# Performance work log

Hardware: AMD Instinct MI355X
Metric: run time of the kernel (lower is better)

The kernel has to match this reference:

```python
import jax, jax.numpy as jnp
import numpy as np

N_NODES = 100000
N_EDGES = 1600000
N_GRAPHS = 256
K_HOPS = 3


def setup_inputs() -> dict:
    key = jax.random.key(0)
    ks = jax.random.split(key, 10)
    x = jax.random.normal(ks[0], (N_NODES, 32), dtype=jnp.float32)
    edge_index = jax.random.randint(ks[1], (2, N_EDGES), 0, N_NODES, dtype=jnp.int32)
    batch = jnp.sort(jax.random.randint(ks[2], (N_NODES,), 0, N_GRAPHS, dtype=jnp.int32))
    gcn_w = jax.random.normal(ks[3], (64, 32), dtype=jnp.float32) * 0.1
    gcn_b = jax.random.normal(ks[4], (64,), dtype=jnp.float32) * 0.1
    w1 = jax.random.normal(ks[5], (32, 64), dtype=jnp.float32) * 0.1
    b1 = jax.random.normal(ks[6], (32,), dtype=jnp.float32) * 0.1
    w2 = jax.random.normal(ks[7], (16, 32), dtype=jnp.float32) * 0.1
    b2 = jax.random.normal(ks[8], (16,), dtype=jnp.float32) * 0.1
    return {"x": x, "edge_index": edge_index, "batch": batch,
            "gcn_w": gcn_w, "gcn_b": gcn_b, "w1": w1, "b1": b1, "w2": w2, "b2": b2}


def reference(x, edge_index, batch, gcn_w, gcn_b, w1, b1, w2, b2):
    N = x.shape[0]
    src, dst = edge_index[0], edge_index[1]
    # GCN symmetric normalization with self-loops: deg = in-degree + 1
    deg = jax.ops.segment_sum(jnp.ones_like(src, dtype=x.dtype), dst, num_segments=N) + 1.0
    norm = deg ** -0.5  # [N]
    h = x
    for _ in range(K_HOPS):
        # edge message: norm[src] * h[src], scattered to dst, scaled by norm[dst];
        # self-loop contributes norm[i]^2 * h[i]
        msg = h[src] * norm[src][:, None]                     # [E, C]
        agg = jax.ops.segment_sum(msg, dst, num_segments=N)    # [N, C]
        h = norm[:, None] * agg + (norm * norm)[:, None] * h
    h = jax.nn.relu(h @ gcn_w.T + gcn_b)                       # [N, hidden]
    # global mean pool per graph
    counts = jax.ops.segment_sum(jnp.ones((N,), x.dtype), batch, num_segments=N_GRAPHS)
    sums = jax.ops.segment_sum(h, batch, num_segments=N_GRAPHS)
    h_avg = sums / jnp.maximum(counts, 1.0)[:, None]           # [G, hidden]
    # classifier (dropout = identity in eval)
    h1 = jax.nn.relu(h_avg @ w1.T + b1)
    logits = h1 @ w2.T + b2                                    # [G, nc]
    return logits
```

## Files before the change

### kernel.cpp

```cpp
#include <hip/hip_runtime.h>

constexpr int NW    = 391;
constexpr int CH    = 8192;
constexpr int CAP_B = 8192;
constexpr int CAP_C = 10240;

__device__ __forceinline__ unsigned bf16_rne(float x) {
    unsigned u = __float_as_uint(x);
    u += 0x7fffu + ((u >> 16) & 1u);
    return u >> 16;
}
__device__ __forceinline__ unsigned pack2(float even, float odd) {
    return bf16_rne(even) | (bf16_rne(odd) << 16);
}
__device__ __forceinline__ float lo_f(unsigned u) { return __uint_as_float(u << 16); }
__device__ __forceinline__ float hi_f(unsigned u) { return __uint_as_float(u & 0xffff0000u); }


__global__ __launch_bounds__(512) void k_bucket(const int* __restrict__ src,
                                                const int* __restrict__ dst, int E,
                                                int* __restrict__ wcur, int* __restrict__ packed) {
    __shared__ int h[256];
    __shared__ int base[256];
    int t = threadIdx.x;
    if (t < 256) h[t] = 0;
    __syncthreads();
    int b0 = blockIdx.x * CH;
    int cnt = min(CH, E - b0);
    if (cnt == CH) {
        const int4* d4 = (const int4*)(dst + b0);
        for (int i = t; i < CH / 4; i += 512) {
            int4 v = d4[i];
            atomicAdd(&h[v.x / NW], 1); atomicAdd(&h[v.y / NW], 1);
            atomicAdd(&h[v.z / NW], 1); atomicAdd(&h[v.w / NW], 1);
        }
    } else {
        for (int i = t; i < cnt; i += 512) atomicAdd(&h[dst[b0 + i] / NW], 1);
    }
    __syncthreads();
    if (t < 256) { base[t] = atomicAdd(&wcur[t], h[t]); h[t] = 0; }
    __syncthreads();
    if (cnt == CH) {
        const int4* d4 = (const int4*)(dst + b0);
        const int4* s4 = (const int4*)(src + b0);
        for (int i = t; i < CH / 4; i += 512) {
            int4 dv = d4[i];
            int4 sv = s4[i];
            int da[4] = {dv.x, dv.y, dv.z, dv.w};
            int sa[4] = {sv.x, sv.y, sv.z, sv.w};
#pragma unroll
            for (int j = 0; j < 4; ++j) {
                int w = da[j] / NW;
                int l = da[j] - w * NW;
                int r = atomicAdd(&h[w], 1);
                int pos = base[w] + r;
                if (pos < CAP_B) packed[w * CAP_B + pos] = (l << 17) | sa[j];
            }
        }
    } else {
        for (int i = t; i < cnt; i += 512) {
            int d = dst[b0 + i];
            int s = src[b0 + i];
            int w = d / NW;
            int l = d - w * NW;
            int r = atomicAdd(&h[w], 1);
            int pos = base[w] + r;
            if (pos < CAP_B) packed[w * CAP_B + pos] = (l << 17) | s;
        }
    }
}


__global__ __launch_bounds__(512) void k_window(const int* __restrict__ packed,
                                                const int* __restrict__ wcur,
                                                const float4* __restrict__ x4,
                                                float* __restrict__ norm,
                                                int2* __restrict__ rng,
                                                int* __restrict__ csr,
                                                uint2* __restrict__ hb, int N, int W) {
    __shared__ int hist[NW];
    __shared__ float snorm[NW];
    __shared__ int pend[NW];
    __shared__ int cur[NW];
    __shared__ int wpart[8];
    int t = threadIdx.x, w = blockIdx.x;
    int lo = w * NW, nwn = min(NW, N - lo);
    for (int i = t; i < NW; i += 512) hist[i] = 0;
    __syncthreads();
    int cnt = min(wcur[w], CAP_B);
    const int* pk = packed + (size_t)w * CAP_B;
    for (int e = t; e < cnt; e += 512) atomicAdd(&hist[pk[e] >> 17], 1);
    __syncthreads();
    int d = (t < nwn) ? hist[t] : 0;
    float nv = rsqrtf((float)(d + 1));
    if (t < nwn) { snorm[t] = nv; norm[lo + t] = nv; }
    int pd = (t < nwn) ? ((d + 7) & ~7) : 0;
    int lane = t & 63, wid = t >> 6;
    int v = pd;
#pragma unroll
    for (int s = 1; s < 64; s <<= 1) {
        int u = __shfl_up(v, s, 64);
        if (lane >= s) v += u;
    }
    if (lane == 63) wpart[wid] = v;
    __syncthreads();
    if (t < 8) {
        int z = wpart[t];
#pragma unroll
        for (int s = 1; s < 8; s <<= 1) {
            int u = __shfl_up(z, s, 8);
            if (t >= s) z += u;
        }
        wpart[t] = z;
    }
    __syncthreads();
    int incl = v + (wid ? wpart[wid - 1] : 0);
    int base = w * CAP_C;
    int cend = base + incl;
    if (t < nwn) {
        rng[lo + t] = make_int2(cend - pd, cend);
        pend[t] = cend;
        cur[t] = cend - pd;
    }
    if (w == W - 1 && t == 0) { norm[N] = 1.f; rng[N] = make_int2(0, 0); }
    __syncthreads();
    for (int e = t; e < cnt; e += 512) {
        int p = pk[e];
        int pos = atomicAdd(&cur[p >> 17], 1);
        csr[pos] = p & 0x1FFFF;
    }
    __syncthreads();
    if (t < nwn) {
        for (int pos = cur[t]; pos < pend[t]; ++pos) csr[pos] = N;
    }
    for (int idx = t; idx < nwn * 8; idx += 512) {
        int node = idx >> 3, q = idx & 7;
        float nn = snorm[node];
        float4 vx = x4[(size_t)(lo + node) * 8 + q];
        hb[(size_t)(lo + node) * 8 + q] =
            make_uint2(pack2(vx.x * nn, vx.y * nn), pack2(vx.z * nn, vx.w * nn));
    }
    if (w == W - 1 && t < 8) hb[(size_t)N * 8 + t] = make_uint2(0u, 0u);
}

template <bool LAST>
__global__ __launch_bounds__(256) void k_hop(const uint4* __restrict__ tab4,
                                             const float* __restrict__ norm,
                                             const int2* __restrict__ rng,
                                             const int* __restrict__ csr,
                                             uint4* __restrict__ out4, int N) {
    int gid = blockIdx.x * blockDim.x + threadIdx.x;
    int group = gid >> 2;
    int l = threadIdx.x & 3;
    if (group > N) return;
    uint4 sv = tab4[(size_t)group * 4 + l];
    float a0 = lo_f(sv.x), a1 = hi_f(sv.x), a2 = lo_f(sv.y), a3 = hi_f(sv.y);
    float a4 = lo_f(sv.z), a5 = hi_f(sv.z), a6 = lo_f(sv.w), a7 = hi_f(sv.w);
    int2 be = rng[group];
    for (int k = be.x; k < be.y; k += 8) {
        int2 ev = *(const int2*)(csr + k + 2 * l);
        uint4 u[8];
#pragma unroll
        for (int j = 0; j < 8; ++j) {
            int s = __shfl((j & 1) ? ev.y : ev.x, j >> 1, 4);
            u[j] = tab4[(size_t)s * 4 + l];
        }
#pragma unroll
        for (int j = 0; j < 8; ++j) {
            a0 += lo_f(u[j].x); a1 += hi_f(u[j].x); a2 += lo_f(u[j].y); a3 += hi_f(u[j].y);
            a4 += lo_f(u[j].z); a5 += hi_f(u[j].z); a6 += lo_f(u[j].w); a7 += hi_f(u[j].w);
        }
    }
    float n = norm[group];
    float sc = LAST ? n : n * n;
    out4[(size_t)group * 4 + l] = make_uint4(pack2(a0 * sc, a1 * sc), pack2(a2 * sc, a3 * sc),
                                             pack2(a4 * sc, a5 * sc), pack2(a6 * sc, a7 * sc));
}


__global__ __launch_bounds__(256) void k_feat(const uint2* __restrict__ hb,
                                              const float* __restrict__ gw,
                                              const float* __restrict__ gb,
                                              uint4* __restrict__ zb4, int N) {
    __shared__ float w[64 * 32];
    __shared__ float bs[64];
    int t = threadIdx.x;
    for (int i = t; i < 64 * 32; i += 256) w[i] = gw[i];
    if (t < 64) bs[t] = gb[t];
    __syncthreads();
    int n = blockIdx.x * 256 + t;
    if (n >= N) return;
    float hrow[32];
    const uint2* hr = hb + (size_t)n * 8;
#pragma unroll
    for (int q = 0; q < 8; ++q) {
        uint2 u = hr[q];
        hrow[q * 4] = lo_f(u.x); hrow[q * 4 + 1] = hi_f(u.x);
        hrow[q * 4 + 2] = lo_f(u.y); hrow[q * 4 + 3] = hi_f(u.y);
    }
#pragma unroll
    for (int c0 = 0; c0 < 64; c0 += 16) {
        float o[16];
#pragma unroll
        for (int cc = 0; cc < 16; ++cc) {
            const float* wr = &w[(c0 + cc) * 32];
            float d = bs[c0 + cc];
#pragma unroll
            for (int k = 0; k < 32; ++k) d += hrow[k] * wr[k];
            o[cc] = fmaxf(d, 0.f);
        }
        zb4[(size_t)n * 8 + (c0 >> 3)] =
            make_uint4(pack2(o[0], o[1]), pack2(o[2], o[3]), pack2(o[4], o[5]), pack2(o[6], o[7]));
        zb4[(size_t)n * 8 + (c0 >> 3) + 1] =
            make_uint4(pack2(o[8], o[9]), pack2(o[10], o[11]), pack2(o[12], o[13]), pack2(o[14], o[15]));
    }
}


__global__ __launch_bounds__(256) void k_pool(const uint2* __restrict__ zb2,
                                              const int* __restrict__ batch, int N,
                                              const float* __restrict__ w1, const float* __restrict__ b1,
                                              const float* __restrict__ w2, const float* __restrict__ b2,
                                              float* __restrict__ out) {
    __shared__ float4 part[16][17];
    __shared__ float havg[64];
    __shared__ float h1s[32];
    __shared__ int se[2];
    int t = threadIdx.x, g = blockIdx.x;
    if (t < 2) {
        int target = g + t;
        int lo = 0, hi = N;
        while (lo < hi) { int mid = (lo + hi) >> 1; if (batch[mid] < target) lo = mid + 1; else hi = mid; }
        se[t] = lo;
    }
    __syncthreads();
    int start = se[0], end = se[1];
    int q = t & 15;
    int r = t >> 4;
    float4 acc = make_float4(0.f, 0.f, 0.f, 0.f);
    for (int n = start + r; n < end; n += 16) {
        uint2 v = zb2[(size_t)n * 16 + q];
        acc.x += lo_f(v.x); acc.y += hi_f(v.x); acc.z += lo_f(v.y); acc.w += hi_f(v.y);
    }
    part[r][q] = acc;
    __syncthreads();
#pragma unroll
    for (int s = 8; s > 0; s >>= 1) {
        if (r < s) {
            float4 a = part[r][q], b = part[r + s][q];
            a.x += b.x; a.y += b.y; a.z += b.z; a.w += b.w;
            part[r][q] = a;
        }
        __syncthreads();
    }
    if (t < 16) {
        int cnt = end - start;
        float inv = 1.f / (float)(cnt > 0 ? cnt : 1);
        float4 a = part[0][t];
        havg[t * 4] = a.x * inv; havg[t * 4 + 1] = a.y * inv;
        havg[t * 4 + 2] = a.z * inv; havg[t * 4 + 3] = a.w * inv;
    }
    __syncthreads();
    if (t < 32) {
        float d = b1[t];
#pragma unroll
        for (int k = 0; k < 64; ++k) d += havg[k] * w1[t * 64 + k];
        h1s[t] = fmaxf(d, 0.f);
    }
    __syncthreads();
    if (t < 16) {
        float d = b2[t];
#pragma unroll
        for (int j = 0; j < 32; ++j) d += h1s[j] * w2[t * 32 + j];
        out[g * 16 + t] = d;
    }
}


extern "C" void kernel_launch(void* const* d_in, const int* in_sizes, int n_in,
                              void* d_out, int out_size, void* d_ws, size_t ws_size,
                              hipStream_t stream) {
    const float* x     = (const float*)d_in[0];
    const int*   ei    = (const int*)d_in[1];
    const int*   batch = (const int*)d_in[2];
    const float* gw    = (const float*)d_in[3];
    const float* gb    = (const float*)d_in[4];
    const float* w1    = (const float*)d_in[5];
    const float* b1    = (const float*)d_in[6];
    const float* w2    = (const float*)d_in[7];
    const float* b2    = (const float*)d_in[8];
    float* out = (float*)d_out;

    int N = in_sizes[2];
    int E = in_sizes[1] / 2;
    int G = out_size / 16;
    const int* srcp = ei;
    const int* dstp = ei + E;

    int W  = (N + NW - 1) / NW;
    int NB = (E + CH - 1) / CH;

    char* ws = (char*)d_ws;
    size_t off = 0;
    auto alloc = [&](size_t bytes) -> void* {
        void* p = ws + off;
        off += (bytes + 255) & ~(size_t)255;
        return p;
    };
    int*   wcur   = (int*)alloc(256 * 4);
    int*   packed = (int*)alloc((size_t)W * CAP_B * 4);
    int*   csr    = (int*)alloc((size_t)W * CAP_C * 4);
    int2*  rng    = (int2*)alloc((size_t)(N + 1) * 8);
    float* norm   = (float*)alloc((size_t)(N + 1) * 4);
    uint2* hbA    = (uint2*)alloc((size_t)(N + 1) * 64);
    uint2* hbB    = (uint2*)alloc((size_t)(N + 1) * 64);
    unsigned* zbuf = (unsigned*)alloc((size_t)N * 64 * 2);

    hipMemsetAsync(wcur, 0, 256 * 4, stream);

    int hb_blocks = ((N + 1) * 4 + 255) / 256;

    k_bucket<<<NB, 512, 0, stream>>>(srcp, dstp, E, wcur, packed);
    k_window<<<W, 512, 0, stream>>>(packed, wcur, (const float4*)x, norm, rng, csr, hbA, N, W);

    k_hop<false><<<hb_blocks, 256, 0, stream>>>((const uint4*)hbA, norm, rng, csr, (uint4*)hbB, N);
    k_hop<false><<<hb_blocks, 256, 0, stream>>>((const uint4*)hbB, norm, rng, csr, (uint4*)hbA, N);
    k_hop<true ><<<hb_blocks, 256, 0, stream>>>((const uint4*)hbA, norm, rng, csr, (uint4*)hbB, N);

    k_feat<<<(N + 255) / 256, 256, 0, stream>>>(hbB, gw, gb, (uint4*)zbuf, N);
    k_pool<<<G, 256, 0, stream>>>((const uint2*)zbuf, batch, N, w1, b1, w2, b2, out);
}
```

Baseline: 211.5 us.

## Use 8 lanes per node in hop gathers and fuse last hop with GCN linear

```diff
diff --git a/kernel.cpp b/kernel.cpp
--- a/kernel.cpp
+++ b/kernel.cpp
@@ -143,76 +143,131 @@
     if (w == W - 1 && t < 8) hb[(size_t)N * 8 + t] = make_uint2(0u, 0u);
 }
 
-template <bool LAST>
-__global__ __launch_bounds__(256) void k_hop(const uint4* __restrict__ tab4,
-                                             const float* __restrict__ norm,
-                                             const int2* __restrict__ rng,
-                                             const int* __restrict__ csr,
-                                             uint4* __restrict__ out4, int N) {
-    int gid = blockIdx.x * blockDim.x + threadIdx.x;
-    int group = gid >> 2;
-    int l = threadIdx.x & 3;
+__global__ void k_hop(const uint2* __restrict__ tab, const float* __restrict__ norm,
+                      const int2* __restrict__ rng, const int* __restrict__ csr,
+                      uint2* __restrict__ outb, int N) {
+    int group = (blockIdx.x * blockDim.x + threadIdx.x) >> 3;
+    int l = threadIdx.x & 7;
     if (group > N) return;
-    uint4 sv = tab4[(size_t)group * 4 + l];
-    float a0 = lo_f(sv.x), a1 = hi_f(sv.x), a2 = lo_f(sv.y), a3 = hi_f(sv.y);
-    float a4 = lo_f(sv.z), a5 = hi_f(sv.z), a6 = lo_f(sv.w), a7 = hi_f(sv.w);
+    uint2 sv = tab[(size_t)group * 8 + l];
+    float ax = lo_f(sv.x), ay = hi_f(sv.x), az = lo_f(sv.y), aw = hi_f(sv.y);
     int2 be = rng[group];
-    for (int k = be.x; k < be.y; k += 8) {
-        int2 ev = *(const int2*)(csr + k + 2 * l);
-        uint4 u[8];
+    int k = be.x;
+    for (; k + 16 <= be.y; k += 16) {
+        int e0 = csr[k + l];
+        int e1 = csr[k + 8 + l];
+        uint2 u[16];
 #pragma unroll
         for (int j = 0; j < 8; ++j) {
-            int s = __shfl((j & 1) ? ev.y : ev.x, j >> 1, 4);
-            u[j] = tab4[(size_t)s * 4 + l];
+            int s = __shfl(e0, j, 8);
+            u[j] = tab[(size_t)s * 8 + l];
         }
 #pragma unroll
         for (int j = 0; j < 8; ++j) {
-            a0 += lo_f(u[j].x); a1 += hi_f(u[j].x); a2 += lo_f(u[j].y); a3 += hi_f(u[j].y);
-            a4 += lo_f(u[j].z); a5 += hi_f(u[j].z); a6 += lo_f(u[j].w); a7 += hi_f(u[j].w);
+            int s = __shfl(e1, j, 8);
+            u[8 + j] = tab[(size_t)s * 8 + l];
+        }
+#pragma unroll
+        for (int j = 0; j < 16; ++j) {
+            ax += lo_f(u[j].x); ay += hi_f(u[j].x);
+            az += lo_f(u[j].y); aw += hi_f(u[j].y);
+        }
+    }
+    if (k < be.y) {
+        int e = csr[k + l];
+        uint2 u[8];
+#pragma unroll
+        for (int j = 0; j < 8; ++j) {
+            int s = __shfl(e, j, 8);
+            u[j] = tab[(size_t)s * 8 + l];
+        }
+#pragma unroll
+        for (int j = 0; j < 8; ++j) {
+            ax += lo_f(u[j].x); ay += hi_f(u[j].x);
+            az += lo_f(u[j].y); aw += hi_f(u[j].y);
         }
     }
     float n = norm[group];
-    float sc = LAST ? n : n * n;
-    out4[(size_t)group * 4 + l] = make_uint4(pack2(a0 * sc, a1 * sc), pack2(a2 * sc, a3 * sc),
-                                             pack2(a4 * sc, a5 * sc), pack2(a6 * sc, a7 * sc));
-}
-
-
-__global__ __launch_bounds__(256) void k_feat(const uint2* __restrict__ hb,
-                                              const float* __restrict__ gw,
-                                              const float* __restrict__ gb,
-                                              uint4* __restrict__ zb4, int N) {
-    __shared__ float w[64 * 32];
+    float sc = n * n;
+    outb[(size_t)group * 8 + l] = make_uint2(pack2(ax * sc, ay * sc), pack2(az * sc, aw * sc));
+}
+
+__global__ __launch_bounds__(256) void k_hopfeat(const uint2* __restrict__ tab,
+                                                 const float* __restrict__ norm,
+                                                 const int2* __restrict__ rng,
+                                                 const int* __restrict__ csr,
+                                                 const float* __restrict__ gw,
+                                                 const float* __restrict__ gb,
+                                                 uint4* __restrict__ zb4, int N) {
+    __shared__ float wT[32][64];
     __shared__ float bs[64];
+    __shared__ float rows[32][33];
     int t = threadIdx.x;
-    for (int i = t; i < 64 * 32; i += 256) w[i] = gw[i];
+    for (int i = t; i < 64 * 32; i += 256) { int c = i >> 5, k = i & 31; wT[k][c] = gw[i]; }
     if (t < 64) bs[t] = gb[t];
-    __syncthreads();
-    int n = blockIdx.x * 256 + t;
-    if (n >= N) return;
-    float hrow[32];
-    const uint2* hr = hb + (size_t)n * 8;
-#pragma unroll
-    for (int q = 0; q < 8; ++q) {
-        uint2 u = hr[q];
-        hrow[q * 4] = lo_f(u.x); hrow[q * 4 + 1] = hi_f(u.x);
-        hrow[q * 4 + 2] = lo_f(u.y); hrow[q * 4 + 3] = hi_f(u.y);
-    }
-#pragma unroll
-    for (int c0 = 0; c0 < 64; c0 += 16) {
-        float o[16];
-#pragma unroll
-        for (int cc = 0; cc < 16; ++cc) {
-            const float* wr = &w[(c0 + cc) * 32];
+    int group = (blockIdx.x * 256 + t) >> 3;
+    int l = t & 7;
+    int node = t >> 3;
+    float ax = 0.f, ay = 0.f, az = 0.f, aw = 0.f;
+    if (group <= N) {
+        uint2 sv = tab[(size_t)group * 8 + l];
+        ax = lo_f(sv.x); ay = hi_f(sv.x); az = lo_f(sv.y); aw = hi_f(sv.y);
+        int2 be = rng[group];
+        int k = be.x;
+        for (; k + 16 <= be.y; k += 16) {
+            int e0 = csr[k + l];
+            int e1 = csr[k + 8 + l];
+            uint2 u[16];
+#pragma unroll
+            for (int j = 0; j < 8; ++j) {
+                int s = __shfl(e0, j, 8);
+                u[j] = tab[(size_t)s * 8 + l];
+            }
+#pragma unroll
+            for (int j = 0; j < 8; ++j) {
+                int s = __shfl(e1, j, 8);
+                u[8 + j] = tab[(size_t)s * 8 + l];
+            }
+#pragma unroll
+            for (int j = 0; j < 16; ++j) {
+                ax += lo_f(u[j].x); ay += hi_f(u[j].x);
+                az += lo_f(u[j].y); aw += hi_f(u[j].y);
+            }
+        }
+        if (k < be.y) {
+            int e = csr[k + l];
+            uint2 u[8];
+#pragma unroll
+            for (int j = 0; j < 8; ++j) {
+                int s = __shfl(e, j, 8);
+                u[j] = tab[(size_t)s * 8 + l];
+            }
+#pragma unroll
+            for (int j = 0; j < 8; ++j) {
+                ax += lo_f(u[j].x); ay += hi_f(u[j].x);
+                az += lo_f(u[j].y); aw += hi_f(u[j].y);
+            }
+        }
+        float n = norm[group];
+        ax *= n; ay *= n; az *= n; aw *= n;
+    }
+    rows[node][l * 4 + 0] = ax;
+    rows[node][l * 4 + 1] = ay;
+    rows[node][l * 4 + 2] = az;
+    rows[node][l * 4 + 3] = aw;
+    __syncthreads();
+    if (group < N) {
+        int c0 = l * 8;
+        float o[8];
+#pragma unroll
+        for (int cc = 0; cc < 8; ++cc) {
             float d = bs[c0 + cc];
 #pragma unroll
-            for (int k = 0; k < 32; ++k) d += hrow[k] * wr[k];
+            for (int k = 0; k < 32; ++k) d += rows[node][k] * wT[k][c0 + cc];
             o[cc] = fmaxf(d, 0.f);
         }
-        zb4[(size_t)n * 8 + (c0 >> 3)] =
+        zb4[(size_t)group * 8 + l] =
             make_uint4(pack2(o[0], o[1]), pack2(o[2], o[3]), pack2(o[4], o[5]), pack2(o[6], o[7]));
-        zb4[(size_t)n * 8 + (c0 >> 3) + 1] =
-            make_uint4(pack2(o[8], o[9]), pack2(o[10], o[11]), pack2(o[12], o[13]), pack2(o[14], o[15]));
     }
 }
 
@@ -318,15 +373,14 @@
 
     hipMemsetAsync(wcur, 0, 256 * 4, stream);
 
-    int hb_blocks = ((N + 1) * 4 + 255) / 256;
+    int pb = ((N + 1) * 8 + 255) / 256;
 
     k_bucket<<<NB, 512, 0, stream>>>(srcp, dstp, E, wcur, packed);
     k_window<<<W, 512, 0, stream>>>(packed, wcur, (const float4*)x, norm, rng, csr, hbA, N, W);
 
-    k_hop<false><<<hb_blocks, 256, 0, stream>>>((const uint4*)hbA, norm, rng, csr, (uint4*)hbB, N);
-    k_hop<false><<<hb_blocks, 256, 0, stream>>>((const uint4*)hbB, norm, rng, csr, (uint4*)hbA, N);
-    k_hop<true ><<<hb_blocks, 256, 0, stream>>>((const uint4*)hbA, norm, rng, csr, (uint4*)hbB, N);
-
-    k_feat<<<(N + 255) / 256, 256, 0, stream>>>(hbB, gw, gb, (uint4*)zbuf, N);
+    k_hop<<<pb, 256, 0, stream>>>(hbA, norm, rng, csr, hbB, N);
+    k_hop<<<pb, 256, 0, stream>>>(hbB, norm, rng, csr, hbA, N);
+    k_hopfeat<<<pb, 256, 0, stream>>>(hbA, norm, rng, csr, gw, gb, (uint4*)zbuf, N);
+
     k_pool<<<G, 256, 0, stream>>>((const uint2*)zbuf, batch, N, w1, b1, w2, b2, out);
 }
```

New measurement: 203.0 us (median of 2 runs). 1.04x faster.
